# Optimization experiments

Measured on AMD Instinct MI355X. Metric: run time of the kernel, lower is better.

Reference implementation:

```python
import jax, jax.numpy as jnp
import numpy as np


def gcn_conv(x, W, b, src, dst, dinv_sqrt, n_nodes):
    # PyG GCNConv: h = X W; out_i = sum_j norm_ij * h_j + b, norm = d_i^-1/2 d_j^-1/2
    h = x @ W  # [N, out]
    norm = dinv_sqrt[src] * dinv_sqrt[dst]  # [E]
    msg = h[src] * norm[:, None]  # [E, out]
    out = jax.ops.segment_sum(msg, dst, num_segments=n_nodes)
    return out + b


def setup_inputs() -> dict:
    key = jax.random.key(0)
    ks = jax.random.split(key, 12)
    N, E, G = 50000, 400000, 512
    x = jax.random.normal(ks[0], (N, 3), dtype=jnp.float32)
    edge_index = jax.random.randint(ks[1], (2, E), 0, N, dtype=jnp.int64)
    batch = jnp.sort(jax.random.randint(ks[2], (N,), 0, G, dtype=jnp.int64))
    def lin(k, fin, fout):
        kw, kb = jax.random.split(k)
        s = 1.0 / np.sqrt(fin)
        return (jax.random.uniform(kw, (fin, fout), jnp.float32, -s, s),
                jax.random.uniform(kb, (fout,), jnp.float32, -s, s))
    W1, b1 = lin(ks[3], 3, 100)
    W2, b2 = lin(ks[4], 100, 200)
    W3, b3 = lin(ks[5], 200, 100)
    W4, b4 = lin(ks[6], 100, 1)
    return {"x": x, "edge_index": edge_index, "batch": batch, "num_graphs": G,
            "W1": W1, "b1": b1, "W2": W2, "b2": b2,
            "W3": W3, "b3": b3, "W4": W4, "b4": b4}


def reference(x, edge_index, batch, num_graphs, W1, b1, W2, b2, W3, b3, W4, b4):
    N = x.shape[0]
    loop = jnp.arange(N, dtype=edge_index.dtype)
    src = jnp.concatenate([edge_index[0], loop])  # self-loops added (GCNConv default)
    dst = jnp.concatenate([edge_index[1], loop])
    deg = jax.ops.segment_sum(jnp.ones_like(src, dtype=x.dtype), dst, num_segments=N)
    dinv_sqrt = deg ** -0.5  # deg >= 1 due to self-loops

    h = jax.nn.silu(gcn_conv(x, W1, b1, src, dst, dinv_sqrt, N))
    h = jax.nn.silu(gcn_conv(h, W2, b2, src, dst, dinv_sqrt, N))

    # global_mean_pool over `batch` segments
    sums = jax.ops.segment_sum(h, batch, num_segments=num_graphs)  # [G, 200]
    cnts = jax.ops.segment_sum(jnp.ones((N,), h.dtype), batch, num_segments=num_graphs)
    pooled = sums / jnp.maximum(cnts, 1.0)[:, None]

    h = jax.nn.silu(pooled @ W3 + b3)
    out = h @ W4 + b4  # [G, 1]
    return out.squeeze(-1)
```

## Files before the change

### kernel.cpp

```cpp
#include <hip/hip_runtime.h>
#include <math.h>

#define WF 64

__device__ __forceinline__ float silu_f(float v){ return v / (1.0f + expf(-v)); }

__global__ __launch_bounds__(256) void k_count(const int* __restrict__ dst, int* __restrict__ cnt, int E){
  int e = blockIdx.x*blockDim.x + threadIdx.x;
  if (e < E) atomicAdd(&cnt[dst[e]], 1);
}

__global__ __launch_bounds__(256) void k_scan1(const int* __restrict__ cnt, int* __restrict__ rowstart, int* __restrict__ bsum, int N){
  __shared__ int s[256];
  int tid = threadIdx.x;
  int base = blockIdx.x*2048 + tid*8;
  int loc[8]; int tsum = 0;
#pragma unroll
  for (int j=0;j<8;++j){ int idx=base+j; int v = (idx<N)?cnt[idx]:0; loc[j]=tsum; tsum+=v; }
  s[tid]=tsum; __syncthreads();
  for (int off=1; off<256; off<<=1){
    int v = (tid>=off)? s[tid-off] : 0;
    __syncthreads();
    s[tid] += v;
    __syncthreads();
  }
  int texc = s[tid] - tsum;
  if (tid==255) bsum[blockIdx.x] = s[255];
#pragma unroll
  for (int j=0;j<8;++j){ int idx=base+j; if (idx<N) rowstart[idx] = texc + loc[j]; }
}

__global__ __launch_bounds__(256) void k_scan3(const int* __restrict__ bsum, const int* __restrict__ cnt,
                        const float* __restrict__ x,
                        int* __restrict__ rowstart, int* __restrict__ cursor,
                        float* __restrict__ dinv, float4* __restrict__ dxp,
                        int N, int E, int nb){
  __shared__ int boffs;
  int tid = threadIdx.x;
  int b = (blockIdx.x*blockDim.x) >> 11;
  if (tid < WF){
    int v = (tid < nb && tid < b) ? bsum[tid] : 0;
#pragma unroll
    for (int off=32; off; off>>=1) v += __shfl_down(v, off);
    if (tid==0) boffs = v;
  }
  __syncthreads();
  int idx = blockIdx.x*blockDim.x + tid;
  if (idx < N){
    int v = rowstart[idx] + boffs;
    rowstart[idx]=v; cursor[idx]=v;
    float di = rsqrtf((float)(cnt[idx]+1));
    dinv[idx] = di;
    float4 o;
    o.x = di;
    o.y = di*x[3*idx+0];
    o.z = di*x[3*idx+1];
    o.w = di*x[3*idx+2];
    dxp[idx] = o;
  }
  if (idx==0) rowstart[N]=E;
}

__global__ __launch_bounds__(256) void k_fill(const int* __restrict__ src, const int* __restrict__ dst,
                       int* __restrict__ cursor, int* __restrict__ colsrc, int E){
  int e = blockIdx.x*blockDim.x + threadIdx.x;
  if (e < E){
    int d = dst[e];
    int pos = atomicAdd(&cursor[d], 1);
    colsrc[pos] = src[e];
  }
}

__global__ __launch_bounds__(256) void k_l1(const float4* __restrict__ dxp,
                     const int* __restrict__ rowstart, const int* __restrict__ colsrc,
                     const float* __restrict__ W1, const float* __restrict__ b1,
                     float* __restrict__ h1s, int N){
  __shared__ float w[300];
  __shared__ float bb[100];
  int tid = threadIdx.x;
  for (int t=tid; t<300; t+=blockDim.x) w[t]=W1[t];
  for (int t=tid; t<100; t+=blockDim.x) bb[t]=b1[t];
  __syncthreads();
  int i = blockIdx.x*blockDim.x + tid;
  if (i >= N) return;
  float4 self = dxp[i];
  float di = self.x;
  float sx = self.y, sy = self.z, sz = self.w;
  int jb = rowstart[i], je = rowstart[i+1];
  int j = jb;
  for (; j+1 < je; j += 2){
    float4 r0 = dxp[colsrc[j]];
    float4 r1 = dxp[colsrc[j+1]];
    sx += r0.y + r1.y; sy += r0.z + r1.z; sz += r0.w + r1.w;
  }
  if (j < je){
    float4 r = dxp[colsrc[j]];
    sx += r.y; sy += r.z; sz += r.w;
  }
  sx*=di; sy*=di; sz*=di;
  float* orow = h1s + (size_t)i*100;
#pragma unroll
  for (int f0=0; f0<100; f0+=4){
    float4 o;
    o.x = silu_f(sx*w[f0+0] + sy*w[100+f0+0] + sz*w[200+f0+0] + bb[f0+0]);
    o.y = silu_f(sx*w[f0+1] + sy*w[100+f0+1] + sz*w[200+f0+1] + bb[f0+1]);
    o.z = silu_f(sx*w[f0+2] + sy*w[100+f0+2] + sz*w[200+f0+2] + bb[f0+2]);
    o.w = silu_f(sx*w[f0+3] + sy*w[100+f0+3] + sz*w[200+f0+3] + bb[f0+3]);
    *(float4*)&orow[f0] = o;
  }
}

__global__ __launch_bounds__(256) void k_agg2(const float* __restrict__ h1s, const int* __restrict__ rowstart,
                       const int* __restrict__ colsrc, const float* __restrict__ dinv,
                       float* __restrict__ a2, int N){
  int node = blockIdx.x*4 + (threadIdx.x >> 6);
  int lane = threadIdx.x & 63;
  if (node >= N || lane >= 50) return;
  float di = dinv[node];
  const float* selfrow = h1s + (size_t)node*100 + 2*lane;
  float2 v = *(const float2*)selfrow;
  float ax = di*v.x, ay = di*v.y;
  int jb = rowstart[node], je = rowstart[node+1];
  int j = jb;
  for (; j+1 < je; j += 2){
    int u0 = colsrc[j];   float w0 = dinv[u0];
    int u1 = colsrc[j+1]; float w1 = dinv[u1];
    float2 r0 = *(const float2*)(h1s + (size_t)u0*100 + 2*lane);
    float2 r1 = *(const float2*)(h1s + (size_t)u1*100 + 2*lane);
    ax += w0*r0.x; ay += w0*r0.y;
    ax += w1*r1.x; ay += w1*r1.y;
  }
  if (j < je){
    int u = colsrc[j]; float wv = dinv[u];
    float2 r = *(const float2*)(h1s + (size_t)u*100 + 2*lane);
    ax += wv*r.x; ay += wv*r.y;
  }
  float2 o; o.x = di*ax; o.y = di*ay;
  *(float2*)(a2 + (size_t)node*100 + 2*lane) = o;
}

#define CH 20
__global__ __launch_bounds__(256, 2) void k_mm2(const float* __restrict__ a2, const float* __restrict__ W2,
                      const float* __restrict__ b2, const int* __restrict__ batch,
                      float* __restrict__ pooled, int N){
  __shared__ float aS[CH][260];
  __shared__ float wS[100][48];
  int tid = threadIdx.x;
  int fg = tid & 3;
  int ng = tid >> 2;
  int n0 = blockIdx.x * 256;
  int fb = blockIdx.y;

  for (int idx = tid; idx < 4000; idx += 256){
    int k = idx / 40, f = idx - k*40;
    int g = f / 10, j = f - g*10;
    wS[k][g*12 + j] = W2[(size_t)k*200 + fb*40 + f];
  }

  float acc[4][10];
#pragma unroll
  for (int i=0;i<4;++i)
#pragma unroll
    for (int j=0;j<10;++j) acc[i][j]=0.f;

  for (int kc = 0; kc < 5; ++kc){
    int kt = kc*CH;
    __syncthreads();
#pragma unroll
    for (int c = 0; c < 5; ++c){
      int idx = c*256 + tid;
      int n = idx / 5, q = idx - n*5;
      int gn = n0 + n;
      float4 v = make_float4(0.f,0.f,0.f,0.f);
      if (gn < N) v = *(const float4*)(a2 + (size_t)gn*100 + kt + q*4);
      aS[q*4+0][n] = v.x;
      aS[q*4+1][n] = v.y;
      aS[q*4+2][n] = v.z;
      aS[q*4+3][n] = v.w;
    }
    __syncthreads();
    float a0[4], w0[10];
    *(float4*)a0 = *(const float4*)&aS[0][ng*4];
    {
      const float* wr = &wS[kt][fg*12];
      *(float4*)&w0[0] = *(const float4*)&wr[0];
      *(float4*)&w0[4] = *(const float4*)&wr[4];
      *(float2*)&w0[8] = *(const float2*)&wr[8];
    }
#pragma unroll
    for (int kl = 0; kl < CH; ++kl){
      float a1r[4], w1r[10];
      if (kl+1 < CH){
        *(float4*)a1r = *(const float4*)&aS[kl+1][ng*4];
        const float* wr = &wS[kt+kl+1][fg*12];
        *(float4*)&w1r[0] = *(const float4*)&wr[0];
        *(float4*)&w1r[4] = *(const float4*)&wr[4];
        *(float2*)&w1r[8] = *(const float2*)&wr[8];
      }
#pragma unroll
      for (int j=0;j<10;++j){
        float wv = w0[j];
#pragma unroll
        for (int i=0;i<4;++i) acc[i][j] += a0[i]*wv;
      }
      if (kl+1 < CH){
#pragma unroll
        for (int i=0;i<4;++i) a0[i] = a1r[i];
#pragma unroll
        for (int j=0;j<10;++j) w0[j] = w1r[j];
      }
    }
  }

  float* plL = &aS[0][0];
  __syncthreads();
  for (int idx = tid; idx < 640; idx += 256) plL[idx] = 0.f;
  __syncthreads();

  int fbase = fb*40 + fg*10;
  float bias[10];
#pragma unroll
  for (int j=0;j<10;++j) bias[j] = b2[fbase+j];
  int g0 = batch[n0];
  float s[10];
  int gprev = -1;
#pragma unroll
  for (int i=0;i<4;++i){
    int n = n0 + ng*4 + i;
    if (n < N){
      int g = batch[n];
      if (g != gprev){
        if (gprev >= 0){
          int dg = gprev - g0;
          if (dg < 16){
#pragma unroll
            for (int j=0;j<10;++j) atomicAdd(&plL[dg*40 + fg*10 + j], s[j]);
          } else {
#pragma unroll
            for (int j=0;j<10;++j) atomicAdd(&pooled[(size_t)gprev*200 + fbase + j], s[j]);
          }
        }
        gprev = g;
#pragma unroll
        for (int j=0;j<10;++j) s[j] = 0.f;
      }
#pragma unroll
      for (int j=0;j<10;++j) s[j] += silu_f(acc[i][j] + bias[j]);
    }
  }
  if (gprev >= 0){
    int dg = gprev - g0;
    if (dg < 16){
#pragma unroll
      for (int j=0;j<10;++j) atomicAdd(&plL[dg*40 + fg*10 + j], s[j]);
    } else {
#pragma unroll
      for (int j=0;j<10;++j) atomicAdd(&pooled[(size_t)gprev*200 + fbase + j], s[j]);
    }
  }
  __syncthreads();
  for (int idx = tid; idx < 640; idx += 256){
    float v = plL[idx];
    if (v != 0.f){
      int r = idx / 40, f = idx - r*40;
      atomicAdd(&pooled[(size_t)(g0+r)*200 + fb*40 + f], v);
    }
  }
}

__global__ __launch_bounds__(256) void k_head(const float* __restrict__ pooled, const int* __restrict__ batch,
                       const float* __restrict__ W3, const float* __restrict__ b3,
                       const float* __restrict__ W4, const float* __restrict__ b4,
                       float* __restrict__ out, int N){
  __shared__ float pl[200];
  __shared__ float h3[100];
  int g = blockIdx.x; int tid = threadIdx.x;
  int lo=0, hi=N;
  while (lo<hi){ int m=(lo+hi)>>1; if (batch[m] < g) lo=m+1; else hi=m; }
  int s = lo;
  hi=N;
  while (lo<hi){ int m=(lo+hi)>>1; if (batch[m] < g+1) lo=m+1; else hi=m; }
  int e = lo;
  float inv = (e>s) ? 1.0f/(float)(e-s) : 0.0f;
  if (tid < 200) pl[tid] = pooled[(size_t)g*200 + tid] * inv;
  __syncthreads();
  if (tid < 100){
    float acc = b3[tid];
    for (int k=0;k<200;++k) acc += pl[k]*W3[k*100+tid];
    h3[tid] = silu_f(acc);
  }
  __syncthreads();
  if (tid < WF){
    float p = 0.f;
    if (tid < 100)      p  = h3[tid]     * W4[tid];
    if (tid + 64 < 100) p += h3[tid+64]  * W4[tid+64];
#pragma unroll
    for (int off=32; off; off>>=1) p += __shfl_down(p, off);
    if (tid==0) out[g] = p + b4[0];
  }
}

extern "C" void kernel_launch(void* const* d_in, const int* in_sizes, int n_in,
                              void* d_out, int out_size, void* d_ws, size_t ws_size,
                              hipStream_t stream){
  const float* x  = (const float*)d_in[0];
  const int*   ei = (const int*)  d_in[1];
  const int* batch= (const int*)  d_in[2];
  const float* W1 = (const float*)d_in[4];
  const float* b1 = (const float*)d_in[5];
  const float* W2 = (const float*)d_in[6];
  const float* b2 = (const float*)d_in[7];
  const float* W3 = (const float*)d_in[8];
  const float* b3 = (const float*)d_in[9];
  const float* W4 = (const float*)d_in[10];
  const float* b4 = (const float*)d_in[11];
  float* out = (float*)d_out;

  int N = in_sizes[0]/3;
  int E = in_sizes[1]/2;
  int G = out_size;
  const int* src = ei;
  const int* dst = ei + E;

  char* base = (char*)d_ws; size_t off = 0;
  auto alloc = [&](size_t bytes)->void*{
    void* p = base + off;
    off = (off + bytes + 255) & ~(size_t)255;
    return p;
  };
  int*   cnt      = (int*)  alloc((size_t)N*4);
  float* pooled   = (float*)alloc((size_t)G*200*4);
  size_t zbytes   = off;
  int*   rowstart = (int*)  alloc((size_t)(N+1)*4);
  int*   cursor   = (int*)  alloc((size_t)N*4);
  int*   bsum     = (int*)  alloc(4096);
  int*   colsrc   = (int*)  alloc((size_t)E*4);
  float* dinv     = (float*)alloc((size_t)N*4);
  float4* dxp     = (float4*)alloc((size_t)N*16);
  float* h1s      = (float*)alloc((size_t)N*100*4);
  float* a2       = (float*)alloc((size_t)N*100*4);
  (void)ws_size; (void)n_in;

  hipMemsetAsync(base, 0, zbytes, stream);
  int gE = (E+255)/256;
  k_count<<<gE,256,0,stream>>>(dst, cnt, E);
  int nb = (N+2047)/2048;
  k_scan1<<<nb,256,0,stream>>>(cnt, rowstart, bsum, N);
  k_scan3<<<(N+255)/256,256,0,stream>>>(bsum, cnt, x, rowstart, cursor, dinv, dxp, N, E, nb);
  k_fill<<<gE,256,0,stream>>>(src, dst, cursor, colsrc, E);
  k_l1<<<(N+255)/256,256,0,stream>>>(dxp, rowstart, colsrc, W1, b1, h1s, N);
  k_agg2<<<(N+3)/4,256,0,stream>>>(h1s, rowstart, colsrc, dinv, a2, N);
  dim3 gmm((N+255)/256, 5);
  k_mm2<<<gmm,256,0,stream>>>(a2, W2, b2, batch, pooled, N);
  k_head<<<G,256,0,stream>>>(pooled, batch, W3, b3, W4, b4, out, N);
}
```

Measured before the change: 184.9 us.

## Widen gather loads in aggregation kernels and simplify mm2 tile staging

```diff
diff --git a/kernel.cpp b/kernel.cpp
--- a/kernel.cpp
+++ b/kernel.cpp
@@ -88,12 +88,16 @@
   float sx = self.y, sy = self.z, sz = self.w;
   int jb = rowstart[i], je = rowstart[i+1];
   int j = jb;
-  for (; j+1 < je; j += 2){
+  for (; j+3 < je; j += 4){
     float4 r0 = dxp[colsrc[j]];
     float4 r1 = dxp[colsrc[j+1]];
-    sx += r0.y + r1.y; sy += r0.z + r1.z; sz += r0.w + r1.w;
-  }
-  if (j < je){
+    float4 r2 = dxp[colsrc[j+2]];
+    float4 r3 = dxp[colsrc[j+3]];
+    sx += (r0.y + r1.y) + (r2.y + r3.y);
+    sy += (r0.z + r1.z) + (r2.z + r3.z);
+    sz += (r0.w + r1.w) + (r2.w + r3.w);
+  }
+  for (; j < je; ++j){
     float4 r = dxp[colsrc[j]];
     sx += r.y; sy += r.z; sz += r.w;
   }
@@ -113,30 +117,42 @@
 __global__ __launch_bounds__(256) void k_agg2(const float* __restrict__ h1s, const int* __restrict__ rowstart,
                        const int* __restrict__ colsrc, const float* __restrict__ dinv,
                        float* __restrict__ a2, int N){
-  int node = blockIdx.x*4 + (threadIdx.x >> 6);
-  int lane = threadIdx.x & 63;
-  if (node >= N || lane >= 50) return;
+  int node = blockIdx.x*8 + (threadIdx.x >> 5);
+  int lane = threadIdx.x & 31;
+  if (node >= N) return;
+  bool act = lane < 25;
   float di = dinv[node];
-  const float* selfrow = h1s + (size_t)node*100 + 2*lane;
-  float2 v = *(const float2*)selfrow;
-  float ax = di*v.x, ay = di*v.y;
+  float4 acc = make_float4(0.f,0.f,0.f,0.f);
+  if (act){
+    float4 v = *(const float4*)(h1s + (size_t)node*100 + lane*4);
+    acc.x = di*v.x; acc.y = di*v.y; acc.z = di*v.z; acc.w = di*v.w;
+  }
   int jb = rowstart[node], je = rowstart[node+1];
   int j = jb;
   for (; j+1 < je; j += 2){
     int u0 = colsrc[j];   float w0 = dinv[u0];
     int u1 = colsrc[j+1]; float w1 = dinv[u1];
-    float2 r0 = *(const float2*)(h1s + (size_t)u0*100 + 2*lane);
-    float2 r1 = *(const float2*)(h1s + (size_t)u1*100 + 2*lane);
-    ax += w0*r0.x; ay += w0*r0.y;
-    ax += w1*r1.x; ay += w1*r1.y;
+    if (act){
+      float4 r0 = *(const float4*)(h1s + (size_t)u0*100 + lane*4);
+      float4 r1 = *(const float4*)(h1s + (size_t)u1*100 + lane*4);
+      acc.x += w0*r0.x + w1*r1.x;
+      acc.y += w0*r0.y + w1*r1.y;
+      acc.z += w0*r0.z + w1*r1.z;
+      acc.w += w0*r0.w + w1*r1.w;
+    }
   }
   if (j < je){
     int u = colsrc[j]; float wv = dinv[u];
-    float2 r = *(const float2*)(h1s + (size_t)u*100 + 2*lane);
-    ax += wv*r.x; ay += wv*r.y;
-  }
-  float2 o; o.x = di*ax; o.y = di*ay;
-  *(float2*)(a2 + (size_t)node*100 + 2*lane) = o;
+    if (act){
+      float4 r = *(const float4*)(h1s + (size_t)u*100 + lane*4);
+      acc.x += wv*r.x; acc.y += wv*r.y; acc.z += wv*r.z; acc.w += wv*r.w;
+    }
+  }
+  if (act){
+    float4 o;
+    o.x = di*acc.x; o.y = di*acc.y; o.z = di*acc.z; o.w = di*acc.w;
+    *(float4*)(a2 + (size_t)node*100 + lane*4) = o;
+  }
 }
 
 #define CH 20
@@ -163,51 +179,36 @@
 #pragma unroll
     for (int j=0;j<10;++j) acc[i][j]=0.f;
 
+  int gn = n0 + tid;
+  bool inb = (gn < N);
+  const float* arow = a2 + (size_t)gn*100;
+
   for (int kc = 0; kc < 5; ++kc){
     int kt = kc*CH;
     __syncthreads();
 #pragma unroll
     for (int c = 0; c < 5; ++c){
-      int idx = c*256 + tid;
-      int n = idx / 5, q = idx - n*5;
-      int gn = n0 + n;
       float4 v = make_float4(0.f,0.f,0.f,0.f);
-      if (gn < N) v = *(const float4*)(a2 + (size_t)gn*100 + kt + q*4);
-      aS[q*4+0][n] = v.x;
-      aS[q*4+1][n] = v.y;
-      aS[q*4+2][n] = v.z;
-      aS[q*4+3][n] = v.w;
+      if (inb) v = *(const float4*)(arow + kt + c*4);
+      aS[c*4+0][tid] = v.x;
+      aS[c*4+1][tid] = v.y;
+      aS[c*4+2][tid] = v.z;
+      aS[c*4+3][tid] = v.w;
     }
     __syncthreads();
-    float a0[4], w0[10];
-    *(float4*)a0 = *(const float4*)&aS[0][ng*4];
-    {
-      const float* wr = &wS[kt][fg*12];
-      *(float4*)&w0[0] = *(const float4*)&wr[0];
-      *(float4*)&w0[4] = *(const float4*)&wr[4];
-      *(float2*)&w0[8] = *(const float2*)&wr[8];
-    }
 #pragma unroll
     for (int kl = 0; kl < CH; ++kl){
-      float a1r[4], w1r[10];
-      if (kl+1 < CH){
-        *(float4*)a1r = *(const float4*)&aS[kl+1][ng*4];
-        const float* wr = &wS[kt+kl+1][fg*12];
-        *(float4*)&w1r[0] = *(const float4*)&wr[0];
-        *(float4*)&w1r[4] = *(const float4*)&wr[4];
-        *(float2*)&w1r[8] = *(const float2*)&wr[8];
-      }
+      float a[4], w[10];
+      *(float4*)a = *(const float4*)&aS[kl][ng*4];
+      const float* wr = &wS[kt+kl][fg*12];
+      *(float4*)&w[0] = *(const float4*)&wr[0];
+      *(float4*)&w[4] = *(const float4*)&wr[4];
+      *(float2*)&w[8] = *(const float2*)&wr[8];
 #pragma unroll
       for (int j=0;j<10;++j){
-        float wv = w0[j];
-#pragma unroll
-        for (int i=0;i<4;++i) acc[i][j] += a0[i]*wv;
-      }
-      if (kl+1 < CH){
-#pragma unroll
-        for (int i=0;i<4;++i) a0[i] = a1r[i];
-#pragma unroll
-        for (int j=0;j<10;++j) w0[j] = w1r[j];
+        float wv = w[j];
+#pragma unroll
+        for (int i=0;i<4;++i) acc[i][j] += a[i]*wv;
       }
     }
   }
@@ -349,7 +350,7 @@
   k_scan3<<<(N+255)/256,256,0,stream>>>(bsum, cnt, x, rowstart, cursor, dinv, dxp, N, E, nb);
   k_fill<<<gE,256,0,stream>>>(src, dst, cursor, colsrc, E);
   k_l1<<<(N+255)/256,256,0,stream>>>(dxp, rowstart, colsrc, W1, b1, h1s, N);
-  k_agg2<<<(N+3)/4,256,0,stream>>>(h1s, rowstart, colsrc, dinv, a2, N);
+  k_agg2<<<(N+7)/8,256,0,stream>>>(h1s, rowstart, colsrc, dinv, a2, N);
   dim3 gmm((N+255)/256, 5);
   k_mm2<<<gmm,256,0,stream>>>(a2, W2, b2, batch, pooled, N);
   k_head<<<G,256,0,stream>>>(pooled, batch, W3, b3, W4, b4, out, N);
```

After: 184.2 us. Within noise of the previous version (-0.4%).
